# Optimization experiments

Measured on AMD Instinct MI355X. Metric: run time of the kernel, lower is better.

## Reference

```python
import jax, jax.numpy as jnp
import numpy as np

B, S, D = 1, 2048, 2048
H, HKV, HD = 16, 8, 128
WINDOW = 1024
EPS = 1e-6
SCALE = HD ** -0.5


def _rope_tables(seq_len, head_dim, theta=10000.0):
    inv_freq = 1.0 / (theta ** (jnp.arange(0, head_dim, 2, dtype=jnp.float32) / head_dim))
    ang = jnp.arange(seq_len, dtype=jnp.float32)[:, None] * inv_freq[None, :]  # [S, hd/2]
    emb = jnp.concatenate([ang, ang], axis=-1)  # [S, hd]
    return jnp.cos(emb)[None], jnp.sin(emb)[None]  # [1, S, hd]


def setup_inputs() -> dict:
    key = jax.random.key(0)
    ks = jax.random.split(key, 8)
    cos, sin = _rope_tables(S, HD)
    return {
        "hidden_states": jax.random.normal(ks[0], (B, S, D), jnp.float32),
        "cos": jnp.broadcast_to(cos, (B, S, HD)),
        "sin": jnp.broadcast_to(sin, (B, S, HD)),
        "Wq": jax.random.normal(ks[1], (D, H * HD), jnp.float32) * (D ** -0.5),
        "Wk": jax.random.normal(ks[2], (D, HKV * HD), jnp.float32) * (D ** -0.5),
        "Wv": jax.random.normal(ks[3], (D, HKV * HD), jnp.float32) * (D ** -0.5),
        "Wo": jax.random.normal(ks[4], (H * HD, D), jnp.float32) * ((H * HD) ** -0.5),
        "q_scale": jax.random.uniform(ks[5], (HD,), jnp.float32, 0.5, 1.5),
        "k_scale": jax.random.uniform(ks[6], (HD,), jnp.float32, 0.5, 1.5),
    }


def _rms_norm(x, scale):
    # per-head RMSNorm over last dim, computed in fp32 (matches RMSNorm module)
    xf = x.astype(jnp.float32)
    var = jnp.mean(xf * xf, axis=-1, keepdims=True)
    return (xf * jax.lax.rsqrt(var + EPS) * scale).astype(x.dtype)


def _rotate_half(x):
    x1, x2 = x[..., : HD // 2], x[..., HD // 2 :]
    return jnp.concatenate([-x2, x1], axis=-1)


def _apply_rope(x, cos, sin):
    # cos/sin: [B,S,hd] -> [B,S,1,hd] (unsqueeze_dim=2)
    c, s = cos[:, :, None, :], sin[:, :, None, :]
    return x * c + _rotate_half(x) * s


def reference(hidden_states, cos, sin, Wq, Wk, Wv, Wo, q_scale, k_scale):
    b, s, _ = hidden_states.shape
    q = (hidden_states @ Wq).reshape(b, s, H, HD)
    k = (hidden_states @ Wk).reshape(b, s, HKV, HD)
    v = (hidden_states @ Wv).reshape(b, s, HKV, HD)
    q = _rms_norm(q, q_scale)
    k = _rms_norm(k, k_scale)
    q = _apply_rope(q, cos, sin)
    k = _apply_rope(k, cos, sin)
    # GQA: repeat kv heads to match query heads (groups are consecutive)
    g = H // HKV
    k = jnp.repeat(k, g, axis=2)  # [b, s, H, hd]
    v = jnp.repeat(v, g, axis=2)
    scores = jnp.einsum("bqhd,bkhd->bhqk", q, k) * SCALE  # [b,H,S,S]
    i = jnp.arange(s)[:, None]
    j = jnp.arange(s)[None, :]
    allowed = (j <= i) & (i - j <= WINDOW)  # causal + sliding window
    scores = jnp.where(allowed[None, None], scores, -jnp.inf)
    attn = jax.nn.softmax(scores, axis=-1)
    out = jnp.einsum("bhqk,bkhd->bqhd", attn, v).reshape(b, s, H * HD)
    return out @ Wo
```

## Files before the change

### kernel.cpp

```cpp
#include <hip/hip_runtime.h>
#include <hip/hip_bf16.h>
#include <cmath>


typedef __bf16 bf16x8 __attribute__((ext_vector_type(8)));
typedef float  f32x4  __attribute__((ext_vector_type(4)));

#define S_LEN    2048
#define NH       16
#define NKV      8
#define HDIM     128
#define WIN      1024
#define QK_SCALE_L2E 0.12751744595f
#define RMS_EPS  1e-6f

__device__ __forceinline__ void gld16(void* lds, const void* g) {
    __builtin_amdgcn_global_load_lds(
        (const __attribute__((address_space(1))) unsigned int*)g,
        (__attribute__((address_space(3))) unsigned int*)lds, 16, 0, 0);
}

__device__ __forceinline__ unsigned short f2bu(float x) {
    __hip_bfloat16 h = __float2bfloat16(x);
    return *(unsigned short*)&h;
}

__global__ __launch_bounds__(256) void trans_cvt_kernel(
    const float* __restrict__ Wq, const float* __restrict__ Wk,
    const float* __restrict__ Wv, const float* __restrict__ Wo,
    const float* __restrict__ hs,
    __hip_bfloat16* __restrict__ WqkvT, __hip_bfloat16* __restrict__ WoT,
    __hip_bfloat16* __restrict__ hsb)
{
    __shared__ __attribute__((aligned(16))) unsigned short tile[64][72];
    int id = blockIdx.x;
    if (id >= 3072) {
        size_t i = ((size_t)(id - 3072) * 256 + threadIdx.x) * 8;
        float4 a = *(const float4*)(hs + i);
        float4 b = *(const float4*)(hs + i + 4);
        unsigned short u[8] = { f2bu(a.x), f2bu(a.y), f2bu(a.z), f2bu(a.w),
                                f2bu(b.x), f2bu(b.y), f2bu(b.z), f2bu(b.w) };
        *(uint4*)(hsb + i) = *(uint4*)u;
        return;
    }
    const float* src; __hip_bfloat16* dst; int N, kt, nt;
    if (id < 1024)      { src = Wq; dst = WqkvT;                          N = 2048; kt = id >> 5;          nt = id & 31; }
    else if (id < 1536) { src = Wk; dst = WqkvT + (size_t)2048*2048;      N = 1024; kt = (id-1024) >> 4;   nt = (id-1024) & 15; }
    else if (id < 2048) { src = Wv; dst = WqkvT + (size_t)3072*2048;      N = 1024; kt = (id-1536) >> 4;   nt = (id-1536) & 15; }
    else                { src = Wo; dst = WoT;                            N = 2048; kt = (id-2048) >> 5;   nt = (id-2048) & 31; }
    int k0 = kt * 64, n0 = nt * 64;
    int tid = threadIdx.x;
#pragma unroll
    for (int p = 0; p < 2; ++p) {
        int c = p*256 + tid; int r = c >> 3, cc = (c & 7) * 8;
        const float* s = src + (size_t)(k0 + r)*N + n0 + cc;
        float4 a = *(const float4*)s;
        float4 b = *(const float4*)(s + 4);
        unsigned short u[8] = { f2bu(a.x), f2bu(a.y), f2bu(a.z), f2bu(a.w),
                                f2bu(b.x), f2bu(b.y), f2bu(b.z), f2bu(b.w) };
        *(uint4*)&tile[r][cc] = *(uint4*)u;
    }
    __syncthreads();
#pragma unroll
    for (int p = 0; p < 2; ++p) {
        int c = p*256 + tid; int r2 = c >> 3, c2 = (c & 7) * 8;
        uint4 o;
        o.x = tile[c2+0][r2] | ((unsigned)tile[c2+1][r2] << 16);
        o.y = tile[c2+2][r2] | ((unsigned)tile[c2+3][r2] << 16);
        o.z = tile[c2+4][r2] | ((unsigned)tile[c2+5][r2] << 16);
        o.w = tile[c2+6][r2] | ((unsigned)tile[c2+7][r2] << 16);
        *(uint4*)(dst + (size_t)(n0 + r2)*2048 + k0 + c2) = o;
    }
}

template <typename OT>
__global__ __launch_bounds__(512, 2) void gemm_bt_256x128_kernel(
    const __hip_bfloat16* __restrict__ A, const __hip_bfloat16* __restrict__ BT,
    OT* __restrict__ C, int M, int N, int K)
{
    __shared__ __attribute__((aligned(16))) __hip_bfloat16 As[2][256*64];
    __shared__ __attribute__((aligned(16))) __hip_bfloat16 Bs[2][128*64];
    const int tid  = threadIdx.x;
    const int lane = tid & 63;
    const int wave = tid >> 6;
    const int quad = lane >> 4, l15 = lane & 15;
    const int m0 = blockIdx.y * 256, n0 = blockIdx.x * 128;
    const int wm = (wave >> 1) * 64;
    const int wn = (wave & 1) * 64;
    const int sw = l15 & 7;

    f32x4 acc[4][4] = {};

    auto stage = [&](int b, int k0) {
#pragma unroll
        for (int p = 0; p < 4; ++p) {
            int L = p*512 + tid;
            int r = L >> 3, s = L & 7;
            int cs = s ^ (r & 7);
            gld16((char*)&As[b][0] + L*16, A + (size_t)(m0 + r)*K + k0 + cs*8);
        }
#pragma unroll
        for (int p = 0; p < 2; ++p) {
            int L = p*512 + tid;
            int r = L >> 3, s = L & 7;
            int cs = s ^ (r & 7);
            gld16((char*)&Bs[b][0] + L*16, BT + (size_t)(n0 + r)*K + k0 + cs*8);
        }
    };

    const int NT = K >> 6;
    stage(0, 0);
    int cur = 0;
    for (int kt = 0; kt < NT; ++kt, cur ^= 1) {
        if (kt + 1 < NT) {
            stage(cur ^ 1, (kt + 1) << 6);
            asm volatile("s_waitcnt vmcnt(6)" ::: "memory");
        } else {
            asm volatile("s_waitcnt vmcnt(0)" ::: "memory");
        }
        __builtin_amdgcn_s_barrier();
        __builtin_amdgcn_sched_barrier(0);
#pragma unroll
        for (int ks = 0; ks < 2; ++ks) {
            const int slot = ((ks*4 + quad) ^ sw) * 8;
            bf16x8 af[4], bfr[4];
#pragma unroll
            for (int t = 0; t < 4; ++t) {
                af[t]  = *(const bf16x8*)(&As[cur][0] + (wm + t*16 + l15)*64 + slot);
                bfr[t] = *(const bf16x8*)(&Bs[cur][0] + (wn + t*16 + l15)*64 + slot);
            }
            __builtin_amdgcn_s_setprio(1);
#pragma unroll
            for (int mt = 0; mt < 4; ++mt)
#pragma unroll
                for (int nt = 0; nt < 4; ++nt)
                    acc[mt][nt] = __builtin_amdgcn_mfma_f32_16x16x32_bf16(af[mt], bfr[nt], acc[mt][nt], 0, 0, 0);
            __builtin_amdgcn_s_setprio(0);
        }
        __builtin_amdgcn_sched_barrier(0);
        __builtin_amdgcn_s_barrier();
    }
#pragma unroll
    for (int mt = 0; mt < 4; ++mt)
#pragma unroll
        for (int nt = 0; nt < 4; ++nt)
#pragma unroll
            for (int r = 0; r < 4; ++r) {
                int row = m0 + wm + mt*16 + quad*4 + r;
                int col = n0 + wn + nt*16 + l15;
                if constexpr (__is_same(OT, float))
                    C[(size_t)row*N + col] = acc[mt][nt][r];
                else
                    C[(size_t)row*N + col] = __float2bfloat16(acc[mt][nt][r]);
            }
}

template <typename OT>
__global__ __launch_bounds__(256, 2) void gemm_bt_kernel(
    const __hip_bfloat16* __restrict__ A, const __hip_bfloat16* __restrict__ BT,
    OT* __restrict__ C, int M, int N, int K)
{
    __shared__ __attribute__((aligned(16))) __hip_bfloat16 As[2][128*64];
    __shared__ __attribute__((aligned(16))) __hip_bfloat16 Bs[2][128*64];
    const int tid  = threadIdx.x;
    const int lane = tid & 63;
    const int wave = tid >> 6;
    const int quad = lane >> 4, l15 = lane & 15;
    const int m0 = blockIdx.y * 128, n0 = blockIdx.x * 128;
    const int wm = (wave >> 1) * 64, wn = (wave & 1) * 64;
    const int sw = l15 & 7;

    f32x4 acc[4][4] = {};

    auto stage = [&](int b, int k0) {
#pragma unroll
        for (int p = 0; p < 4; ++p) {
            int L = p*256 + tid;
            int r = L >> 3, s = L & 7;
            int cs = s ^ (r & 7);
            gld16((char*)&As[b][0] + L*16, A + (size_t)(m0 + r)*K + k0 + cs*8);
        }
#pragma unroll
        for (int p = 0; p < 4; ++p) {
            int L = p*256 + tid;
            int r = L >> 3, s = L & 7;
            int cs = s ^ (r & 7);
            gld16((char*)&Bs[b][0] + L*16, BT + (size_t)(n0 + r)*K + k0 + cs*8);
        }
    };

    const int NT = K >> 6;
    stage(0, 0);
    int cur = 0;
    for (int kt = 0; kt < NT; ++kt, cur ^= 1) {
        __syncthreads();
        if (kt + 1 < NT) stage(cur ^ 1, (kt + 1) << 6);
#pragma unroll
        for (int ks = 0; ks < 2; ++ks) {
            const int slot = ((ks*4 + quad) ^ sw) * 8;
            bf16x8 af[4], bfr[4];
#pragma unroll
            for (int t = 0; t < 4; ++t) {
                af[t]  = *(const bf16x8*)(&As[cur][0] + (wm + t*16 + l15)*64 + slot);
                bfr[t] = *(const bf16x8*)(&Bs[cur][0] + (wn + t*16 + l15)*64 + slot);
            }
#pragma unroll
            for (int mt = 0; mt < 4; ++mt)
#pragma unroll
                for (int nt = 0; nt < 4; ++nt)
                    acc[mt][nt] = __builtin_amdgcn_mfma_f32_16x16x32_bf16(af[mt], bfr[nt], acc[mt][nt], 0, 0, 0);
        }
    }
#pragma unroll
    for (int mt = 0; mt < 4; ++mt)
#pragma unroll
        for (int nt = 0; nt < 4; ++nt)
#pragma unroll
            for (int r = 0; r < 4; ++r) {
                int row = m0 + wm + mt*16 + quad*4 + r;
                int col = n0 + wn + nt*16 + l15;
                if constexpr (__is_same(OT, float))
                    C[(size_t)row*N + col] = acc[mt][nt][r];
                else
                    C[(size_t)row*N + col] = __float2bfloat16(acc[mt][nt][r]);
            }
}

__global__ __launch_bounds__(256) void rms_vt_kernel(
    const __hip_bfloat16* __restrict__ qkv,
    const float* __restrict__ cosb, const float* __restrict__ sinb,
    const float* __restrict__ qsc,  const float* __restrict__ ksc,
    __hip_bfloat16* __restrict__ Qn, __hip_bfloat16* __restrict__ Kn,
    __hip_bfloat16* __restrict__ Vt)
{
    __shared__ __attribute__((aligned(16))) unsigned short tile[64][72];
    int id = blockIdx.x;
    if (id >= 2048) {
        int t  = id - 2048;
        int s0 = (t & 31) * 64;
        int v0 = (t >> 5) * 64;
        int tid = threadIdx.x;
#pragma unroll
        for (int p = 0; p < 2; ++p) {
            int c = p*256 + tid; int r = c >> 3, cc = (c & 7) * 8;
            uint4 v = *(const uint4*)(qkv + (size_t)(s0 + r)*4096 + 3072 + v0 + cc);
            *(uint4*)&tile[r][cc] = v;
        }
        __syncthreads();
#pragma unroll
        for (int p = 0; p < 2; ++p) {
            int c = p*256 + tid; int r2 = c >> 3, c2 = (c & 7) * 8;
            uint4 o;
            o.x = tile[c2+0][r2] | ((unsigned)tile[c2+1][r2] << 16);
            o.y = tile[c2+2][r2] | ((unsigned)tile[c2+3][r2] << 16);
            o.z = tile[c2+4][r2] | ((unsigned)tile[c2+5][r2] << 16);
            o.w = tile[c2+6][r2] | ((unsigned)tile[c2+7][r2] << 16);
            *(uint4*)(Vt + (size_t)(v0 + r2)*2048 + s0 + c2) = o;
        }
        return;
    }
    int s = id;
    int wave = threadIdx.x >> 6, lane = threadIdx.x & 63;
    float c1 = cosb[s*128 + lane];
    float c2 = cosb[s*128 + 64 + lane];
    float s1 = sinb[s*128 + lane];
    float s2 = sinb[s*128 + 64 + lane];
    for (int u = wave; u < 24; u += 4) {
        bool isq = (u < 16);
        int h = isq ? u : u - 16;
        const __hip_bfloat16* x = qkv + (size_t)s*4096 + (isq ? h*128 : 2048 + h*128);
        float x1 = (float)x[lane], x2 = (float)x[lane + 64];
        float ss = x1*x1 + x2*x2;
#pragma unroll
        for (int off = 32; off; off >>= 1) ss += __shfl_xor(ss, off);
        float r = rsqrtf(ss * (1.0f/128.0f) + RMS_EPS);
        if (isq) r *= QK_SCALE_L2E;
        const float* sc = isq ? qsc : ksc;
        float y1 = x1 * r * sc[lane];
        float y2 = x2 * r * sc[lane + 64];
        float o1 = y1*c1 - y2*s1;
        float o2 = y2*c2 + y1*s2;
        __hip_bfloat16* dst = isq ? (Qn + (size_t)s*2048 + h*128)
                                  : (Kn + (size_t)s*1024 + h*128);
        dst[lane]      = __float2bfloat16(o1);
        dst[lane + 64] = __float2bfloat16(o2);
    }
}

__global__ __launch_bounds__(256, 2) void attn_kernel(
    const __hip_bfloat16* __restrict__ Qn,
    const __hip_bfloat16* __restrict__ Kn,
    const __hip_bfloat16* __restrict__ Vt,
    __hip_bfloat16* __restrict__ O)
{
    __shared__ __attribute__((aligned(16))) __hip_bfloat16 Ksm[2][64*128];
    __shared__ __attribute__((aligned(16))) __hip_bfloat16 Vsm[2][128*64];
    __shared__ __attribute__((aligned(16))) __hip_bfloat16 P[4][16][76];

    const int bx   = blockIdx.x;
    const int h    = bx & 15;
    const int qb   = 31 - (bx >> 4);
    const int i0   = qb * 64;
    const int hk   = h >> 1;
    const int tid  = threadIdx.x, wave = tid >> 6, lane = tid & 63;
    const int quad = lane >> 4, l15 = lane & 15;
    const int ib   = i0 + wave * 16;

    const __hip_bfloat16* Kh = Kn + hk * HDIM;
    const __hip_bfloat16* Vh = Vt + (size_t)(hk * HDIM) * 2048;

    bf16x8 qf[4];
    const __hip_bfloat16* qbase = Qn + (size_t)(ib + l15)*2048 + h*HDIM + quad*8;
#pragma unroll
    for (int kk = 0; kk < 4; ++kk) qf[kk] = *(const bf16x8*)(qbase + kk*32);

    f32x4 o[8] = {};
    float lrow[4] = {0.f, 0.f, 0.f, 0.f};

    int j_lo = i0 - WIN; if (j_lo < 0) j_lo = 0;
    const int jstart = j_lo & ~63;
    const int jend   = i0;

    auto stage = [&](int b, int j0) {
#pragma unroll
        for (int p = 0; p < 4; ++p) {
            int L = p*256 + tid;
            int r = L >> 4;
            int c = (L & 15) ^ (r & 15);
            gld16((char*)&Ksm[b][0] + L*16, Kh + (size_t)(j0 + r)*1024 + c*8);
        }
#pragma unroll
        for (int p = 0; p < 4; ++p) {
            int L = p*256 + tid;
            int dv = L >> 3;
            int c = (L & 7) ^ (dv & 7);
            gld16((char*)&Vsm[b][0] + L*16, Vh + (size_t)dv*2048 + j0 + c*8);
        }
    };

    stage(0, jstart);
    int cur = 0;
    for (int j0 = jstart; j0 <= jend; j0 += 64, cur ^= 1) {
        __syncthreads();
        if (j0 + 64 <= jend) stage(cur ^ 1, j0 + 64);

        f32x4 sacc[4] = {};
#pragma unroll
        for (int nt = 0; nt < 4; ++nt) {
            const int r = nt*16 + l15;
#pragma unroll
            for (int kk = 0; kk < 4; ++kk) {
                const int cc = (kk*4 + quad) ^ l15;
                bf16x8 kfr = *(const bf16x8*)(&Ksm[cur][0] + r*128 + cc*8);
                sacc[nt] = __builtin_amdgcn_mfma_f32_16x16x32_bf16(qf[kk], kfr, sacc[nt], 0, 0, 0);
            }
        }

        const bool need_mask = (j0 + 63 > ib) || (j0 < ib + 15 - WIN);
        if (need_mask) {
#pragma unroll
            for (int nt = 0; nt < 4; ++nt) {
                int j = j0 + nt*16 + l15;
#pragma unroll
                for (int r = 0; r < 4; ++r) {
                    int i = ib + quad*4 + r;
                    bool valid = (j <= i) && (i - j <= WIN);
                    float p = valid ? __builtin_exp2f(sacc[nt][r]) : 0.f;
                    lrow[r] += p;
                    P[wave][quad*4 + r][nt*16 + l15] = __float2bfloat16(p);
                }
            }
        } else {
#pragma unroll
            for (int nt = 0; nt < 4; ++nt)
#pragma unroll
                for (int r = 0; r < 4; ++r) {
                    float p = __builtin_exp2f(sacc[nt][r]);
                    lrow[r] += p;
                    P[wave][quad*4 + r][nt*16 + l15] = __float2bfloat16(p);
                }
        }

#pragma unroll
        for (int ks = 0; ks < 2; ++ks) {
            bf16x8 pf = *(const bf16x8*)&P[wave][l15][ks*32 + quad*8];
#pragma unroll
            for (int dt = 0; dt < 8; ++dt) {
                const int dv = dt*16 + l15;
                const int cc = (ks*4 + quad) ^ (l15 & 7);
                bf16x8 vfr = *(const bf16x8*)(&Vsm[cur][0] + dv*64 + cc*8);
                o[dt] = __builtin_amdgcn_mfma_f32_16x16x32_bf16(pf, vfr, o[dt], 0, 0, 0);
            }
        }
    }

#pragma unroll
    for (int r = 0; r < 4; ++r) {
        lrow[r] += __shfl_xor(lrow[r], 1);
        lrow[r] += __shfl_xor(lrow[r], 2);
        lrow[r] += __shfl_xor(lrow[r], 4);
        lrow[r] += __shfl_xor(lrow[r], 8);
        float inv = 1.0f / lrow[r];
        int row = ib + quad*4 + r;
#pragma unroll
        for (int dt = 0; dt < 8; ++dt)
            O[(size_t)row*2048 + h*HDIM + dt*16 + l15] = __float2bfloat16(o[dt][r] * inv);
    }
}

extern "C" void kernel_launch(void* const* d_in, const int* in_sizes, int n_in,
                              void* d_out, int out_size, void* d_ws, size_t ws_size,
                              hipStream_t stream)
{
    (void)in_sizes; (void)n_in; (void)out_size; (void)ws_size;
    const float* hs   = (const float*)d_in[0];
    const float* cosb = (const float*)d_in[1];
    const float* sinb = (const float*)d_in[2];
    const float* Wq   = (const float*)d_in[3];
    const float* Wk   = (const float*)d_in[4];
    const float* Wv   = (const float*)d_in[5];
    const float* Wo   = (const float*)d_in[6];
    const float* qs   = (const float*)d_in[7];
    const float* ks   = (const float*)d_in[8];

    char* ws = (char*)d_ws;
    __hip_bfloat16* WqkvT = (__hip_bfloat16*)(ws);
    __hip_bfloat16* WoT   = (__hip_bfloat16*)(ws + (16u << 20));
    __hip_bfloat16* QKV   = (__hip_bfloat16*)(ws + (24u << 20));
    __hip_bfloat16* Qn    = (__hip_bfloat16*)(ws + (40u << 20));
    __hip_bfloat16* Kn    = (__hip_bfloat16*)(ws + (48u << 20));
    __hip_bfloat16* Vt    = (__hip_bfloat16*)(ws + (52u << 20));
    __hip_bfloat16* hsb   = (__hip_bfloat16*)(ws + (56u << 20));
    __hip_bfloat16* AT    = (__hip_bfloat16*)(ws + (56u << 20));

    trans_cvt_kernel<<<dim3(5120), dim3(256), 0, stream>>>(Wq, Wk, Wv, Wo, hs, WqkvT, WoT, hsb);
    gemm_bt_256x128_kernel<__hip_bfloat16><<<dim3(32, 8), dim3(512), 0, stream>>>(hsb, WqkvT, QKV, 2048, 4096, 2048);
    rms_vt_kernel<<<dim3(2560), dim3(256), 0, stream>>>(QKV, cosb, sinb, qs, ks, Qn, Kn, Vt);
    attn_kernel<<<dim3(512), dim3(256), 0, stream>>>(Qn, Kn, Vt, AT);
    gemm_bt_kernel<float><<<dim3(16, 16), dim3(256), 0, stream>>>(AT, WoT, (float*)d_out, 2048, 2048, 2048);
}
```

Measured before the change: 237.3 us.

## Fuse RMSNorm, RoPE and V transpose into QKV GEMM epilogue

The QKV projection GEMM now writes its accumulator tile into LDS and, in the epilogue, applies per-head RMSNorm, scaling and RoPE for Q/K tiles, or transposes V tiles directly into Vt. This removes the separate rms_vt kernel and the intermediate bf16 QKV buffer round-trip through global memory. The GEMM tile changes from 256x128 with 512 threads to 128x128 with 256 threads, and the explicit vmcnt-based pipelining and setprio hints are replaced by a plain __syncthreads double buffer. That could make the main loop less efficient.

```diff
diff --git a/kernel.cpp b/kernel.cpp
--- a/kernel.cpp
+++ b/kernel.cpp
@@ -73,20 +73,23 @@
     }
 }
 
-template <typename OT>
-__global__ __launch_bounds__(512, 2) void gemm_bt_256x128_kernel(
-    const __hip_bfloat16* __restrict__ A, const __hip_bfloat16* __restrict__ BT,
-    OT* __restrict__ C, int M, int N, int K)
+__global__ __launch_bounds__(256, 2) void gemm_qkv_kernel(
+    const __hip_bfloat16* __restrict__ A,
+    const __hip_bfloat16* __restrict__ BT,
+    const float* __restrict__ cosb, const float* __restrict__ sinb,
+    const float* __restrict__ qsc,  const float* __restrict__ ksc,
+    __hip_bfloat16* __restrict__ Qn, __hip_bfloat16* __restrict__ Kn,
+    __hip_bfloat16* __restrict__ Vt)
 {
-    __shared__ __attribute__((aligned(16))) __hip_bfloat16 As[2][256*64];
+    __shared__ __attribute__((aligned(16))) __hip_bfloat16 As[2][128*64];
     __shared__ __attribute__((aligned(16))) __hip_bfloat16 Bs[2][128*64];
+    const int K = 2048;
     const int tid  = threadIdx.x;
     const int lane = tid & 63;
     const int wave = tid >> 6;
     const int quad = lane >> 4, l15 = lane & 15;
-    const int m0 = blockIdx.y * 256, n0 = blockIdx.x * 128;
-    const int wm = (wave >> 1) * 64;
-    const int wn = (wave & 1) * 64;
+    const int m0 = blockIdx.y * 128, n0 = blockIdx.x * 128;
+    const int wm = (wave >> 1) * 64, wn = (wave & 1) * 64;
     const int sw = l15 & 7;
 
     f32x4 acc[4][4] = {};
@@ -94,14 +97,14 @@
     auto stage = [&](int b, int k0) {
 #pragma unroll
         for (int p = 0; p < 4; ++p) {
-            int L = p*512 + tid;
+            int L = p*256 + tid;
             int r = L >> 3, s = L & 7;
             int cs = s ^ (r & 7);
             gld16((char*)&As[b][0] + L*16, A + (size_t)(m0 + r)*K + k0 + cs*8);
         }
 #pragma unroll
-        for (int p = 0; p < 2; ++p) {
-            int L = p*512 + tid;
+        for (int p = 0; p < 4; ++p) {
+            int L = p*256 + tid;
             int r = L >> 3, s = L & 7;
             int cs = s ^ (r & 7);
             gld16((char*)&Bs[b][0] + L*16, BT + (size_t)(n0 + r)*K + k0 + cs*8);
@@ -112,14 +115,8 @@
     stage(0, 0);
     int cur = 0;
     for (int kt = 0; kt < NT; ++kt, cur ^= 1) {
-        if (kt + 1 < NT) {
-            stage(cur ^ 1, (kt + 1) << 6);
-            asm volatile("s_waitcnt vmcnt(6)" ::: "memory");
-        } else {
-            asm volatile("s_waitcnt vmcnt(0)" ::: "memory");
-        }
-        __builtin_amdgcn_s_barrier();
-        __builtin_amdgcn_sched_barrier(0);
+        __syncthreads();
+        if (kt + 1 < NT) stage(cur ^ 1, (kt + 1) << 6);
 #pragma unroll
         for (int ks = 0; ks < 2; ++ks) {
             const int slot = ((ks*4 + quad) ^ sw) * 8;
@@ -129,30 +126,95 @@
                 af[t]  = *(const bf16x8*)(&As[cur][0] + (wm + t*16 + l15)*64 + slot);
                 bfr[t] = *(const bf16x8*)(&Bs[cur][0] + (wn + t*16 + l15)*64 + slot);
             }
-            __builtin_amdgcn_s_setprio(1);
 #pragma unroll
             for (int mt = 0; mt < 4; ++mt)
 #pragma unroll
                 for (int nt = 0; nt < 4; ++nt)
                     acc[mt][nt] = __builtin_amdgcn_mfma_f32_16x16x32_bf16(af[mt], bfr[nt], acc[mt][nt], 0, 0, 0);
-            __builtin_amdgcn_s_setprio(0);
-        }
-        __builtin_amdgcn_sched_barrier(0);
-        __builtin_amdgcn_s_barrier();
-    }
-#pragma unroll
-    for (int mt = 0; mt < 4; ++mt)
-#pragma unroll
-        for (int nt = 0; nt < 4; ++nt)
-#pragma unroll
-            for (int r = 0; r < 4; ++r) {
-                int row = m0 + wm + mt*16 + quad*4 + r;
-                int col = n0 + wn + nt*16 + l15;
-                if constexpr (__is_same(OT, float))
-                    C[(size_t)row*N + col] = acc[mt][nt][r];
-                else
-                    C[(size_t)row*N + col] = __float2bfloat16(acc[mt][nt][r]);
-            }
+        }
+    }
+
+    const int kind = (n0 < 2048) ? 0 : (n0 < 3072) ? 1 : 2;
+
+    __syncthreads();
+    unsigned short* ep = (unsigned short*)&As[0][0];
+
+    if (kind == 2) {
+#pragma unroll
+        for (int mt = 0; mt < 4; ++mt)
+#pragma unroll
+            for (int nt = 0; nt < 4; ++nt)
+#pragma unroll
+                for (int r = 0; r < 4; ++r) {
+                    int row = wm + mt*16 + quad*4 + r;
+                    int col = wn + nt*16 + l15;
+                    ep[col*128 + (((row>>3) ^ (col&7))<<3) + (row&7)] = f2bu(acc[mt][nt][r]);
+                }
+    } else {
+#pragma unroll
+        for (int mt = 0; mt < 4; ++mt)
+#pragma unroll
+            for (int nt = 0; nt < 4; ++nt)
+#pragma unroll
+                for (int r = 0; r < 4; ++r) {
+                    int row = wm + mt*16 + quad*4 + r;
+                    int col = wn + nt*16 + l15;
+                    ep[row*128 + (((col>>3) ^ (row&7))<<3) + (col&7)] = f2bu(acc[mt][nt][r]);
+                }
+    }
+    __syncthreads();
+
+    auto ldchunk = [&](int ri, int j) -> bf16x8 {
+        return *(const bf16x8*)(ep + ri*128 + ((j ^ (ri & 7)) << 3));
+    };
+
+    const int r  = tid >> 1;
+    const int hf = tid & 1;
+
+    if (kind == 2) {
+        const int v0 = n0 - 3072;
+        __hip_bfloat16* outp = Vt + (size_t)(v0 + r)*2048 + m0 + hf*64;
+#pragma unroll
+        for (int j = 0; j < 8; ++j) {
+            bf16x8 c = ldchunk(r, hf*8 + j);
+            *(bf16x8*)(outp + 8*j) = c;
+        }
+    } else {
+        const int s = m0 + r;
+        const bool isq = (kind == 0);
+        const int h   = isq ? (n0 >> 7) : ((n0 - 2048) >> 7);
+        float ss = 0.f;
+#pragma unroll
+        for (int j = 0; j < 8; ++j) {
+            bf16x8 c = ldchunk(r, hf*8 + j);
+#pragma unroll
+            for (int i = 0; i < 8; ++i) { float x = (float)c[i]; ss += x*x; }
+        }
+        ss += __shfl_xor(ss, 1);
+        float rr = rsqrtf(ss * (1.0f/128.0f) + RMS_EPS);
+        if (isq) rr *= QK_SCALE_L2E;
+        const float* sc = isq ? qsc : ksc;
+        __hip_bfloat16* outbase = isq ? (Qn + (size_t)s*2048 + h*128)
+                                      : (Kn + (size_t)s*1024 + h*128);
+        const float* crow = cosb + (size_t)s*128;
+        const float* srow = sinb + (size_t)s*128;
+#pragma unroll
+        for (int j = 0; j < 8; ++j) {
+            bf16x8 xa = ldchunk(r, j);
+            bf16x8 xb = ldchunk(r, j + 8);
+            const int dout = hf*64 + 8*j;
+            unsigned short out[8];
+#pragma unroll
+            for (int i = 0; i < 8; ++i) {
+                float y1 = (float)xa[i] * rr * sc[8*j + i];
+                float y2 = (float)xb[i] * rr * sc[64 + 8*j + i];
+                float cv = crow[dout + i], sv = srow[dout + i];
+                float o  = (hf == 0) ? (y1*cv - y2*sv) : (y2*cv + y1*sv);
+                out[i] = f2bu(o);
+            }
+            *(uint4*)(outbase + dout) = *(uint4*)out;
+        }
+    }
 }
 
 template <typename OT>
@@ -226,67 +288,6 @@
             }
 }
 
-__global__ __launch_bounds__(256) void rms_vt_kernel(
-    const __hip_bfloat16* __restrict__ qkv,
-    const float* __restrict__ cosb, const float* __restrict__ sinb,
-    const float* __restrict__ qsc,  const float* __restrict__ ksc,
-    __hip_bfloat16* __restrict__ Qn, __hip_bfloat16* __restrict__ Kn,
-    __hip_bfloat16* __restrict__ Vt)
-{
-    __shared__ __attribute__((aligned(16))) unsigned short tile[64][72];
-    int id = blockIdx.x;
-    if (id >= 2048) {
-        int t  = id - 2048;
-        int s0 = (t & 31) * 64;
-        int v0 = (t >> 5) * 64;
-        int tid = threadIdx.x;
-#pragma unroll
-        for (int p = 0; p < 2; ++p) {
-            int c = p*256 + tid; int r = c >> 3, cc = (c & 7) * 8;
-            uint4 v = *(const uint4*)(qkv + (size_t)(s0 + r)*4096 + 3072 + v0 + cc);
-            *(uint4*)&tile[r][cc] = v;
-        }
-        __syncthreads();
-#pragma unroll
-        for (int p = 0; p < 2; ++p) {
-            int c = p*256 + tid; int r2 = c >> 3, c2 = (c & 7) * 8;
-            uint4 o;
-            o.x = tile[c2+0][r2] | ((unsigned)tile[c2+1][r2] << 16);
-            o.y = tile[c2+2][r2] | ((unsigned)tile[c2+3][r2] << 16);
-            o.z = tile[c2+4][r2] | ((unsigned)tile[c2+5][r2] << 16);
-            o.w = tile[c2+6][r2] | ((unsigned)tile[c2+7][r2] << 16);
-            *(uint4*)(Vt + (size_t)(v0 + r2)*2048 + s0 + c2) = o;
-        }
-        return;
-    }
-    int s = id;
-    int wave = threadIdx.x >> 6, lane = threadIdx.x & 63;
-    float c1 = cosb[s*128 + lane];
-    float c2 = cosb[s*128 + 64 + lane];
-    float s1 = sinb[s*128 + lane];
-    float s2 = sinb[s*128 + 64 + lane];
-    for (int u = wave; u < 24; u += 4) {
-        bool isq = (u < 16);
-        int h = isq ? u : u - 16;
-        const __hip_bfloat16* x = qkv + (size_t)s*4096 + (isq ? h*128 : 2048 + h*128);
-        float x1 = (float)x[lane], x2 = (float)x[lane + 64];
-        float ss = x1*x1 + x2*x2;
-#pragma unroll
-        for (int off = 32; off; off >>= 1) ss += __shfl_xor(ss, off);
-        float r = rsqrtf(ss * (1.0f/128.0f) + RMS_EPS);
-        if (isq) r *= QK_SCALE_L2E;
-        const float* sc = isq ? qsc : ksc;
-        float y1 = x1 * r * sc[lane];
-        float y2 = x2 * r * sc[lane + 64];
-        float o1 = y1*c1 - y2*s1;
-        float o2 = y2*c2 + y1*s2;
-        __hip_bfloat16* dst = isq ? (Qn + (size_t)s*2048 + h*128)
-                                  : (Kn + (size_t)s*1024 + h*128);
-        dst[lane]      = __float2bfloat16(o1);
-        dst[lane + 64] = __float2bfloat16(o2);
-    }
-}
-
 __global__ __launch_bounds__(256, 2) void attn_kernel(
     const __hip_bfloat16* __restrict__ Qn,
     const __hip_bfloat16* __restrict__ Kn,
@@ -426,7 +427,6 @@
     char* ws = (char*)d_ws;
     __hip_bfloat16* WqkvT = (__hip_bfloat16*)(ws);
     __hip_bfloat16* WoT   = (__hip_bfloat16*)(ws + (16u << 20));
-    __hip_bfloat16* QKV   = (__hip_bfloat16*)(ws + (24u << 20));
     __hip_bfloat16* Qn    = (__hip_bfloat16*)(ws + (40u << 20));
     __hip_bfloat16* Kn    = (__hip_bfloat16*)(ws + (48u << 20));
     __hip_bfloat16* Vt    = (__hip_bfloat16*)(ws + (52u << 20));
@@ -434,8 +434,7 @@
     __hip_bfloat16* AT    = (__hip_bfloat16*)(ws + (56u << 20));
 
     trans_cvt_kernel<<<dim3(5120), dim3(256), 0, stream>>>(Wq, Wk, Wv, Wo, hs, WqkvT, WoT, hsb);
-    gemm_bt_256x128_kernel<__hip_bfloat16><<<dim3(32, 8), dim3(512), 0, stream>>>(hsb, WqkvT, QKV, 2048, 4096, 2048);
-    rms_vt_kernel<<<dim3(2560), dim3(256), 0, stream>>>(QKV, cosb, sinb, qs, ks, Qn, Kn, Vt);
+    gemm_qkv_kernel<<<dim3(32, 16), dim3(256), 0, stream>>>(hsb, WqkvT, cosb, sinb, qs, ks, Qn, Kn, Vt);
     attn_kernel<<<dim3(512), dim3(256), 0, stream>>>(Qn, Kn, Vt, AT);
     gemm_bt_kernel<float><<<dim3(16, 16), dim3(256), 0, stream>>>(AT, WoT, (float*)d_out, 2048, 2048, 2048);
 }
```

After: 240.2 us. Within noise of the previous version (+1.2%).
